# Kernel optimization log

Measured on AMD Instinct MI355X. Metric: run time of the kernel, lower is better.

## Reference

```python
import jax, jax.numpy as jnp
import numpy as np

VOCAB = 50257
D_MODEL = 768
N_LAYERS = 4
N_HEADS = 12
D_HEAD = D_MODEL // N_HEADS
MAX_LEN = 5000
EPS = 1e-5


def _make_pe(max_len, d_model):
    # sinusoidal PE, interleaved sin/cos, base n=10000 (matches PositionalEncodingLayer)
    pos = jnp.arange(max_len, dtype=jnp.float32)[:, None]            # [L,1]
    i = jnp.arange(d_model // 2, dtype=jnp.float32)[None, :]         # [1,D/2]
    theta = pos / jnp.power(10000.0, 2.0 * i / d_model)              # [L,D/2]
    pe = jnp.zeros((max_len, d_model), dtype=jnp.float32)
    pe = pe.at[:, 0::2].set(jnp.sin(theta))
    pe = pe.at[:, 1::2].set(jnp.cos(theta))
    return pe


def setup_inputs() -> dict:
    key = jax.random.key(0)
    ks = jax.random.split(key, 10)
    B, S = 2, 1024
    tokens = jax.random.randint(ks[0], (B, S), 0, VOCAB)
    std = 0.02
    embed = jax.random.normal(ks[1], (VOCAB, D_MODEL), jnp.float32) * std
    pe = _make_pe(MAX_LEN, D_MODEL)
    # per-layer stacked params, torch nn.Linear convention: y = x @ W.T + b
    wq_w = jax.random.normal(ks[2], (N_LAYERS, D_MODEL, D_MODEL), jnp.float32) * std
    wk_w = jax.random.normal(ks[3], (N_LAYERS, D_MODEL, D_MODEL), jnp.float32) * std
    wv_w = jax.random.normal(ks[4], (N_LAYERS, D_MODEL, D_MODEL), jnp.float32) * std
    lin_w = jax.random.normal(ks[5], (N_LAYERS, D_MODEL, D_MODEL), jnp.float32) * std
    wq_b = jnp.zeros((N_LAYERS, D_MODEL), jnp.float32)
    wk_b = jnp.zeros((N_LAYERS, D_MODEL), jnp.float32)
    wv_b = jnp.zeros((N_LAYERS, D_MODEL), jnp.float32)
    lin_b = jnp.zeros((N_LAYERS, D_MODEL), jnp.float32)
    n1_s = jnp.ones((N_LAYERS, D_MODEL), jnp.float32)
    n1_b = jnp.zeros((N_LAYERS, D_MODEL), jnp.float32)
    n2_s = jnp.ones((N_LAYERS, D_MODEL), jnp.float32)
    n2_b = jnp.zeros((N_LAYERS, D_MODEL), jnp.float32)
    unembed_w = jax.random.normal(ks[6], (VOCAB, D_MODEL), jnp.float32) * std
    unembed_b = jnp.zeros((VOCAB,), jnp.float32)
    return dict(tokens=tokens, embed=embed, pe=pe,
                wq_w=wq_w, wq_b=wq_b, wk_w=wk_w, wk_b=wk_b, wv_w=wv_w, wv_b=wv_b,
                lin_w=lin_w, lin_b=lin_b, n1_s=n1_s, n1_b=n1_b, n2_s=n2_s, n2_b=n2_b,
                unembed_w=unembed_w, unembed_b=unembed_b)


def _layernorm(x, scale, bias):
    m = jnp.mean(x, axis=-1, keepdims=True)
    v = jnp.mean(jnp.square(x - m), axis=-1, keepdims=True)
    return (x - m) * jax.lax.rsqrt(v + EPS) * scale + bias


def _attn_block(x, wq_w, wq_b, wk_w, wk_b, wv_w, wv_b, lin_w, lin_b, n1_s, n1_b, n2_s, n2_b):
    B, S, D = x.shape
    def proj(w, b):
        y = x @ w.T + b
        return y.reshape(B, S, N_HEADS, D_HEAD).transpose(0, 2, 1, 3)  # [B,H,S,Dh]
    q, k, v = proj(wq_w, wq_b), proj(wk_w, wk_b), proj(wv_w, wv_b)
    scores = jnp.einsum('bhqd,bhkd->bhqk', q, k) / jnp.sqrt(jnp.float32(D_HEAD))
    causal = jnp.tril(jnp.ones((S, S), dtype=bool))
    scores = jnp.where(causal, scores, -jnp.inf)
    probs = jax.nn.softmax(scores, axis=-1)
    attn = jnp.einsum('bhqk,bhkd->bhqd', probs, v)
    attn = attn.transpose(0, 2, 1, 3).reshape(B, S, D)
    x = _layernorm(x + attn, n1_s, n1_b)
    x = _layernorm(x + (x @ lin_w.T + lin_b), n2_s, n2_b)
    return x


def reference(tokens, embed, pe, wq_w, wq_b, wk_w, wk_b, wv_w, wv_b,
              lin_w, lin_b, n1_s, n1_b, n2_s, n2_b, unembed_w, unembed_b):
    B, S = tokens.shape
    x = embed[tokens] + pe[:S]
    for l in range(N_LAYERS):
        x = _attn_block(x, wq_w[l], wq_b[l], wk_w[l], wk_b[l], wv_w[l], wv_b[l],
                        lin_w[l], lin_b[l], n1_s[l], n1_b[l], n2_s[l], n2_b[l])
    logits = x @ unembed_w.T + unembed_b
    return logits
```

## Files before the change

### kernel.cpp

```cpp
#include <hip/hip_runtime.h>
#include <hip/hip_bf16.h>


#define VOCAB 50257
#define DM 768
#define NL 4
#define NH 12
#define DH 64
#define SEQ 1024
#define BATCH 2
#define ROWS (BATCH * SEQ)
#define QKVN (3 * DM)

typedef __attribute__((ext_vector_type(8))) short short8;
typedef __attribute__((ext_vector_type(4))) float f32x4;

__device__ __forceinline__ unsigned short f2bf(float f) {
    union { float f; unsigned u; } v; v.f = f;
    unsigned r = v.u + 0x7FFFu + ((v.u >> 16) & 1u);
    return (unsigned short)(r >> 16);
}

#define GLOAD16(gp, lp)                                                        \
    __builtin_amdgcn_global_load_lds(                                          \
        (const __attribute__((address_space(1))) unsigned int*)(gp),           \
        (__attribute__((address_space(3))) unsigned int*)(lp), 16, 0, 0)

__global__ __launch_bounds__(256) void cvt_kernel(const float* __restrict__ in,
                                                  unsigned short* __restrict__ out,
                                                  int n4) {
    int i = blockIdx.x * 256 + threadIdx.x;
    if (i < n4) {
        float4 v = ((const float4*)in)[i];
        ushort4 o;
        o.x = f2bf(v.x); o.y = f2bf(v.y); o.z = f2bf(v.z); o.w = f2bf(v.w);
        ((ushort4*)out)[i] = o;
    }
}

__global__ __launch_bounds__(256) void cvt_qkv_kernel(const float* __restrict__ wq,
                                                      const float* __restrict__ wk,
                                                      const float* __restrict__ wv,
                                                      unsigned short* __restrict__ dst,
                                                      int n4) {
    int i = blockIdx.x * 256 + threadIdx.x;
    if (i >= n4) return;
    const int PER_L = 3 * DM * DM / 4, PER_W = DM * DM / 4;
    int l = i / PER_L;
    int rem = i - l * PER_L;
    int w = rem / PER_W;
    int r2 = rem - w * PER_W;
    const float* src = (w == 0) ? wq : (w == 1) ? wk : wv;
    float4 v = ((const float4*)src)[(size_t)l * PER_W + r2];
    ushort4 o;
    o.x = f2bf(v.x); o.y = f2bf(v.y); o.z = f2bf(v.z); o.w = f2bf(v.w);
    ((ushort4*)dst)[i] = o;
}

__global__ __launch_bounds__(256) void pack_qkv_bias(const float* __restrict__ bq,
                                                     const float* __restrict__ bk,
                                                     const float* __restrict__ bv,
                                                     float* __restrict__ dst) {
    int i = blockIdx.x * 256 + threadIdx.x;
    if (i >= NL * QKVN) return;
    int l = i / QKVN, c = i - l * QKVN;
    int w = c / DM, cc = c - w * DM;
    const float* src = (w == 0) ? bq : (w == 1) ? bk : bv;
    dst[i] = src[l * DM + cc];
}

__global__ __launch_bounds__(256) void embed_kernel(const int* __restrict__ tok,
                                                    const float* __restrict__ emb,
                                                    const float* __restrict__ pe,
                                                    float* __restrict__ xf,
                                                    unsigned short* __restrict__ xb) {
    int row = blockIdx.x;
    int t = tok[row];
    int s = row & (SEQ - 1);
    #pragma unroll
    for (int j = 0; j < 3; ++j) {
        int c = threadIdx.x + j * 256;
        float v = emb[(size_t)t * DM + c] + pe[(size_t)s * DM + c];
        xf[(size_t)row * DM + c] = v;
        xb[(size_t)row * DM + c] = f2bf(v);
    }
}

__device__ __forceinline__ float block_sum(float x, float* red) {
    #pragma unroll
    for (int off = 32; off > 0; off >>= 1) x += __shfl_down(x, off);
    int w = threadIdx.x >> 6;
    if ((threadIdx.x & 63) == 0) red[w] = x;
    __syncthreads();
    float t = (red[0] + red[1]) + (red[2] + red[3]);
    __syncthreads();
    return t;
}

__global__ __launch_bounds__(256) void ln_kernel(const float* __restrict__ A,
                                                 const float* __restrict__ Bi,
                                                 const float* __restrict__ sc,
                                                 const float* __restrict__ bi,
                                                 float* __restrict__ xf,
                                                 unsigned short* __restrict__ xb) {
    __shared__ float red[4];
    int row = blockIdx.x, tid = threadIdx.x;
    const float* ap = A + (size_t)row * DM;
    const float* bp = Bi + (size_t)row * DM;
    float v[3], sum = 0.f;
    #pragma unroll
    for (int j = 0; j < 3; ++j) { v[j] = ap[tid + j * 256] + bp[tid + j * 256]; sum += v[j]; }
    sum = block_sum(sum, red);
    float mean = sum * (1.f / DM);
    float vs = 0.f;
    #pragma unroll
    for (int j = 0; j < 3; ++j) { float d = v[j] - mean; vs += d * d; }
    vs = block_sum(vs, red);
    float rstd = rsqrtf(vs * (1.f / DM) + 1e-5f);
    #pragma unroll
    for (int j = 0; j < 3; ++j) {
        int c = tid + j * 256;
        float o = (v[j] - mean) * rstd * sc[c] + bi[c];
        xf[(size_t)row * DM + c] = o;
        xb[(size_t)row * DM + c] = f2bf(o);
    }
}

template <int OUT_BF16>
__global__ __launch_bounds__(256) void gemm128(const unsigned short* __restrict__ A,
                                               const unsigned short* __restrict__ B,
                                               const float* __restrict__ bias,
                                               void* __restrict__ C,
                                               int M, int N, int K, int gx) {
    __shared__ __align__(16) unsigned short As[128 * 64];
    __shared__ __align__(16) unsigned short Bs[128 * 64];
    int bid = blockIdx.x;
    const int nwg = gridDim.x;
    if ((nwg & 7) == 0) {
        int q = nwg >> 3;
        bid = (bid & 7) * q + (bid >> 3);
    }
    const int bx = bid % gx, by = bid / gx;
    const int m0 = bx * 128, n0 = by * 128;
    const int tid = threadIdx.x, lane = tid & 63, wid = tid >> 6;
    const int wm = wid >> 1, wn = wid & 1;
    const int lr = lane & 15, lq = lane >> 4;

    const int sr = wid * 32 + (lane >> 3);
    const int sch = lane & 7;
    const int scs = sch ^ (sr & 7);
    const unsigned short* aP[4];
    const unsigned short* bP[4];
    unsigned short* aL[4];
    unsigned short* bL[4];
    #pragma unroll
    for (int i = 0; i < 4; ++i) {
        int r = sr + i * 8;
        aP[i] = A + (size_t)(m0 + r) * K + scs * 8;
        int br = n0 + r; if (br >= N) br = N - 1;
        bP[i] = B + (size_t)br * K + scs * 8;
        aL[i] = &As[r * 64 + sch * 8];
        bL[i] = &Bs[r * 64 + sch * 8];
    }

    f32x4 acc[4][4] = {};

    for (int k0 = 0; k0 < K; k0 += 64) {
        #pragma unroll
        for (int i = 0; i < 4; ++i) GLOAD16(aP[i] + k0, aL[i]);
        #pragma unroll
        for (int i = 0; i < 4; ++i) GLOAD16(bP[i] + k0, bL[i]);
        __syncthreads();
        #pragma unroll
        for (int kk = 0; kk < 2; ++kk) {
            short8 a[4], b[4];
            #pragma unroll
            for (int i = 0; i < 4; ++i) {
                int ar = wm * 64 + i * 16 + lr;
                a[i] = *reinterpret_cast<const short8*>(
                    &As[ar * 64 + (((kk * 4 + lq) ^ (ar & 7)) * 8)]);
                int br = wn * 64 + i * 16 + lr;
                b[i] = *reinterpret_cast<const short8*>(
                    &Bs[br * 64 + (((kk * 4 + lq) ^ (br & 7)) * 8)]);
            }
            #pragma unroll
            for (int i = 0; i < 4; ++i)
                #pragma unroll
                for (int j = 0; j < 4; ++j)
                    acc[i][j] = __builtin_amdgcn_mfma_f32_16x16x32_bf16(a[i], b[j], acc[i][j], 0, 0, 0);
        }
        __syncthreads();
    }
    #pragma unroll
    for (int i = 0; i < 4; ++i) {
        int row = m0 + wm * 64 + i * 16 + lq * 4;
        #pragma unroll
        for (int j = 0; j < 4; ++j) {
            int col = n0 + wn * 64 + j * 16 + lr;
            if (col < N) {
                float bv = bias[col];
                #pragma unroll
                for (int r = 0; r < 4; ++r) {
                    float v = acc[i][j][r] + bv;
                    if (OUT_BF16) ((unsigned short*)C)[(size_t)(row + r) * N + col] = f2bf(v);
                    else          ((float*)C)[(size_t)(row + r) * N + col] = v;
                }
            }
        }
    }
}

__global__ __launch_bounds__(256) void attn_kernel(const unsigned short* __restrict__ Q,
                                                   const unsigned short* __restrict__ K,
                                                   const unsigned short* __restrict__ V,
                                                   int ld,
                                                   float* __restrict__ O) {
    __shared__ __align__(16) unsigned short Ks[64 * 64];
    __shared__ __align__(16) unsigned short Vs[64 * 64];
    __shared__ __align__(16) unsigned short Ps[4][16 * 64];
    const int qb = blockIdx.x;
    const int bh = blockIdx.y;
    const int b = bh / NH, h = bh % NH;
    const int tid = threadIdx.x, lane = tid & 63, w = tid >> 6;
    const int lr = lane & 15, lq = lane >> 4;
    const int wq0 = qb * 64 + w * 16;
    const size_t base = (size_t)b * SEQ * ld + h * DH;
    const size_t obase = (size_t)b * SEQ * DM + h * DH;

    short8 qf[2];
    {
        const unsigned short* qp = Q + base + (size_t)(wq0 + lr) * ld + lq * 8;
        qf[0] = *reinterpret_cast<const short8*>(qp);
        qf[1] = *reinterpret_cast<const short8*>(qp + 32);
    }
    f32x4 o_acc[4] = {};
    float mrow[4], lrow[4];
    #pragma unroll
    for (int r = 0; r < 4; ++r) { mrow[r] = -1e30f; lrow[r] = 0.f; }

    const int srow = tid >> 3, scol = (tid & 7) * 8;
    for (int t = 0; t <= qb; ++t) {
        const int kv0 = t * 64;
        #pragma unroll
        for (int rr = 0; rr < 2; ++rr) {
            int row = rr * 32 + srow;
            {
                const unsigned short* kp = K + base + (size_t)(kv0 + row) * ld + scol;
                short8 v = *reinterpret_cast<const short8*>(kp);
                *reinterpret_cast<short8*>(&Ks[(row * 64 + scol) ^ ((row & 7) << 3)]) = v;
            }
            {
                const unsigned short* vp = V + base + (size_t)(kv0 + row) * ld + scol;
                short8 v = *reinterpret_cast<const short8*>(vp);
                #pragma unroll
                for (int j = 0; j < 8; ++j) {
                    int d = scol + j;
                    Vs[(d * 64 + row) ^ ((d & 7) << 3)] = (unsigned short)v[j];
                }
            }
        }
        __syncthreads();
        if (kv0 <= wq0 + 15) {
            f32x4 s[4];
            #pragma unroll
            for (int n = 0; n < 4; ++n) {
                int br = n * 16 + lr;
                short8 b0 = *reinterpret_cast<const short8*>(&Ks[(br * 64 + lq * 8) ^ ((br & 7) << 3)]);
                short8 b1 = *reinterpret_cast<const short8*>(&Ks[(br * 64 + 32 + lq * 8) ^ ((br & 7) << 3)]);
                f32x4 z = {};
                z = __builtin_amdgcn_mfma_f32_16x16x32_bf16(qf[0], b0, z, 0, 0, 0);
                z = __builtin_amdgcn_mfma_f32_16x16x32_bf16(qf[1], b1, z, 0, 0, 0);
                s[n] = z;
            }
            const bool diag = (t == qb);
            #pragma unroll
            for (int n = 0; n < 4; ++n)
                #pragma unroll
                for (int r = 0; r < 4; ++r) {
                    float v = s[n][r] * 0.125f;
                    if (diag) {
                        int rg = wq0 + lq * 4 + r;
                        int cg = kv0 + n * 16 + lr;
                        if (cg > rg) v = -1e30f;
                    }
                    s[n][r] = v;
                }
            float f[4];
            #pragma unroll
            for (int r = 0; r < 4; ++r) {
                float mx = fmaxf(fmaxf(s[0][r], s[1][r]), fmaxf(s[2][r], s[3][r]));
                #pragma unroll
                for (int off = 1; off < 16; off <<= 1) mx = fmaxf(mx, __shfl_xor(mx, off));
                float mn = fmaxf(mrow[r], mx);
                f[r] = exp2f((mrow[r] - mn) * 1.44269504f);
                mrow[r] = mn;
            }
            #pragma unroll
            for (int n = 0; n < 4; ++n)
                #pragma unroll
                for (int r = 0; r < 4; ++r)
                    s[n][r] = exp2f((s[n][r] - mrow[r]) * 1.44269504f);
            #pragma unroll
            for (int r = 0; r < 4; ++r) {
                float ls = ((s[0][r] + s[1][r]) + (s[2][r] + s[3][r]));
                #pragma unroll
                for (int off = 1; off < 16; off <<= 1) ls += __shfl_xor(ls, off);
                lrow[r] = lrow[r] * f[r] + ls;
            }
            #pragma unroll
            for (int n = 0; n < 4; ++n)
                #pragma unroll
                for (int r = 0; r < 4; ++r) {
                    int pr = lq * 4 + r, pc = n * 16 + lr;
                    Ps[w][(pr * 64 + pc) ^ ((pr & 7) << 3)] = f2bf(s[n][r]);
                }
            #pragma unroll
            for (int n = 0; n < 4; ++n)
                #pragma unroll
                for (int r = 0; r < 4; ++r) o_acc[n][r] *= f[r];
            #pragma unroll
            for (int kk = 0; kk < 2; ++kk) {
                short8 pa = *reinterpret_cast<const short8*>(
                    &Ps[w][(lr * 64 + kk * 32 + lq * 8) ^ ((lr & 7) << 3)]);
                #pragma unroll
                for (int n = 0; n < 4; ++n) {
                    int vr = n * 16 + lr;
                    short8 bv = *reinterpret_cast<const short8*>(
                        &Vs[(vr * 64 + kk * 32 + lq * 8) ^ ((vr & 7) << 3)]);
                    o_acc[n] = __builtin_amdgcn_mfma_f32_16x16x32_bf16(pa, bv, o_acc[n], 0, 0, 0);
                }
            }
        }
        __syncthreads();
    }
    #pragma unroll
    for (int r = 0; r < 4; ++r) {
        float inv = 1.f / lrow[r];
        int row = wq0 + lq * 4 + r;
        #pragma unroll
        for (int n = 0; n < 4; ++n)
            O[obase + (size_t)row * DM + n * 16 + lr] = o_acc[n][r] * inv;
    }
}

extern "C" void kernel_launch(void* const* d_in, const int* in_sizes, int n_in,
                              void* d_out, int out_size, void* d_ws, size_t ws_size,
                              hipStream_t stream) {
    const int*   tokens   = (const int*)d_in[0];
    const float* embed    = (const float*)d_in[1];
    const float* pe       = (const float*)d_in[2];
    const float* wq_w     = (const float*)d_in[3];
    const float* wq_b     = (const float*)d_in[4];
    const float* wk_w     = (const float*)d_in[5];
    const float* wk_b     = (const float*)d_in[6];
    const float* wv_w     = (const float*)d_in[7];
    const float* wv_b     = (const float*)d_in[8];
    const float* lin_w    = (const float*)d_in[9];
    const float* lin_b    = (const float*)d_in[10];
    const float* n1_s     = (const float*)d_in[11];
    const float* n1_b     = (const float*)d_in[12];
    const float* n2_s     = (const float*)d_in[13];
    const float* n2_b     = (const float*)d_in[14];
    const float* unemb_w  = (const float*)d_in[15];
    const float* unemb_b  = (const float*)d_in[16];

    char* ws = (char*)d_ws;
    size_t off = 0;
    auto carve = [&](size_t bytes) { char* p = ws + off; off += (bytes + 255) & ~(size_t)255; return p; };
    float*          xf     = (float*)carve((size_t)ROWS * DM * 4);
    float*          yb     = (float*)carve((size_t)ROWS * DM * 4);
    unsigned short* xb     = (unsigned short*)carve((size_t)ROWS * DM * 2);
    unsigned short* qkv    = (unsigned short*)carve((size_t)ROWS * QKVN * 2);
    unsigned short* wqkv_h = (unsigned short*)carve((size_t)NL * QKVN * DM * 2);
    unsigned short* lin_h  = (unsigned short*)carve((size_t)NL * DM * DM * 2);
    unsigned short* ue_h   = (unsigned short*)carve((size_t)VOCAB * DM * 2);
    float*          qkvb   = (float*)carve((size_t)NL * QKVN * 4);

    {
        int nq4 = NL * QKVN * DM / 4;
        cvt_qkv_kernel<<<(nq4 + 255) / 256, 256, 0, stream>>>(wq_w, wk_w, wv_w, wqkv_h, nq4);
        int nl4 = NL * DM * DM / 4;
        cvt_kernel<<<(nl4 + 255) / 256, 256, 0, stream>>>(lin_w, lin_h, nl4);
        int nu4 = VOCAB * DM / 4;
        cvt_kernel<<<(nu4 + 255) / 256, 256, 0, stream>>>(unemb_w, ue_h, nu4);
        pack_qkv_bias<<<(NL * QKVN + 255) / 256, 256, 0, stream>>>(wq_b, wk_b, wv_b, qkvb);
    }
    embed_kernel<<<ROWS, 256, 0, stream>>>(tokens, embed, pe, xf, xb);

    const int gx = ROWS / 128;
    for (int l = 0; l < NL; ++l) {
        gemm128<1><<<gx * (QKVN / 128), 256, 0, stream>>>(
            xb, wqkv_h + (size_t)l * QKVN * DM, qkvb + l * QKVN, qkv,
            ROWS, QKVN, DM, gx);
        attn_kernel<<<dim3(SEQ / 64, BATCH * NH), 256, 0, stream>>>(
            qkv, qkv + DM, qkv + 2 * DM, QKVN, yb);
        ln_kernel<<<ROWS, 256, 0, stream>>>(xf, yb, n1_s + l * DM, n1_b + l * DM, xf, xb);
        gemm128<0><<<gx * (DM / 128), 256, 0, stream>>>(
            xb, lin_h + (size_t)l * DM * DM, lin_b + l * DM, yb,
            ROWS, DM, DM, gx);
        ln_kernel<<<ROWS, 256, 0, stream>>>(xf, yb, n2_s + l * DM, n2_b + l * DM, xf, xb);
    }
    const int gyu = (VOCAB + 127) / 128;
    gemm128<0><<<gx * gyu, 256, 0, stream>>>(
        xb, ue_h, unemb_b, (float*)d_out, ROWS, VOCAB, DM, gx);
}
```

Before: 809.3 us.

## Use 256x256-tile, 512-thread GEMM for the unembedding projection

Adds a gemm256 kernel with 256x256 output tiles, 8 waves, double-buffered LDS staging through global_load_lds, and XOR-swizzled LDS reads. It replaces the 128x128 gemm128 launch for the large vocab logits GEMM. Larger tiles raise arithmetic intensity and cut redundant A/B loads on the dominant GEMM. In exchange the kernel uses 128KB of LDS and many accumulator registers, which limits occupancy, and the last N tile wastes more work at the vocab edge.

```diff
diff --git a/kernel.cpp b/kernel.cpp
--- a/kernel.cpp
+++ b/kernel.cpp
@@ -208,6 +208,111 @@
             }
         }
     }
+}
+
+template <int OUT_BF16>
+__global__ __launch_bounds__(512, 2) void gemm256(const unsigned short* __restrict__ A,
+                                                  const unsigned short* __restrict__ B,
+                                                  const float* __restrict__ bias,
+                                                  void* __restrict__ C,
+                                                  int M, int N, int K, int gx) {
+    __shared__ __align__(16) unsigned short As[2][256 * 64];
+    __shared__ __align__(16) unsigned short Bs[2][256 * 64];
+    int bid = blockIdx.x;
+    const int nwg = gridDim.x;
+    if ((nwg & 7) == 0) { int q = nwg >> 3; bid = (bid & 7) * q + (bid >> 3); }
+    const int bx = bid % gx, by = bid / gx;
+    const int m0 = bx * 256, n0 = by * 256;
+    const int tid = threadIdx.x, lane = tid & 63, wid = tid >> 6;
+    const int wm = wid >> 2, wn = wid & 3;
+    const int lr = lane & 15, lq = lane >> 4;
+
+    const int sr = tid >> 3;
+    const int sch = tid & 7;
+    const int scs = sch ^ (sr & 7);
+    const unsigned short* aP[4];
+    const unsigned short* bP[4];
+    #pragma unroll
+    for (int i = 0; i < 4; ++i) {
+        int r = sr + i * 64;
+        aP[i] = A + (size_t)(m0 + r) * K + scs * 8;
+        int br = n0 + r; if (br >= N) br = N - 1;
+        bP[i] = B + (size_t)br * K + scs * 8;
+    }
+
+    #define STAGE256(kt, c)                                                    \
+        do {                                                                   \
+            const int _ko = (kt) * 64;                                         \
+            _Pragma("unroll")                                                  \
+            for (int _i = 0; _i < 4; ++_i)                                     \
+                GLOAD16(aP[_i] + _ko, &As[c][(sr + _i * 64) * 64 + sch * 8]);  \
+            _Pragma("unroll")                                                  \
+            for (int _i = 0; _i < 4; ++_i)                                     \
+                GLOAD16(bP[_i] + _ko, &Bs[c][(sr + _i * 64) * 64 + sch * 8]);  \
+        } while (0)
+
+    f32x4 acc[8][4] = {};
+    const int NT = K >> 6;
+
+    STAGE256(0, 0);
+    STAGE256(1, 1);
+    asm volatile("s_waitcnt vmcnt(8)" ::: "memory");
+    __builtin_amdgcn_s_barrier();
+
+    for (int kt = 0; kt < NT; ++kt) {
+        const int c = kt & 1;
+        #pragma unroll
+        for (int kk = 0; kk < 2; ++kk) {
+            short8 af[8], bf[4];
+            #pragma unroll
+            for (int i = 0; i < 8; ++i) {
+                int ar = wm * 128 + i * 16 + lr;
+                af[i] = *reinterpret_cast<const short8*>(
+                    &As[c][ar * 64 + (((kk * 4 + lq) ^ (ar & 7)) * 8)]);
+            }
+            #pragma unroll
+            for (int j = 0; j < 4; ++j) {
+                int br = wn * 64 + j * 16 + lr;
+                bf[j] = *reinterpret_cast<const short8*>(
+                    &Bs[c][br * 64 + (((kk * 4 + lq) ^ (br & 7)) * 8)]);
+            }
+            __builtin_amdgcn_s_setprio(1);
+            #pragma unroll
+            for (int i = 0; i < 8; ++i)
+                #pragma unroll
+                for (int j = 0; j < 4; ++j)
+                    acc[i][j] = __builtin_amdgcn_mfma_f32_16x16x32_bf16(af[i], bf[j], acc[i][j], 0, 0, 0);
+            __builtin_amdgcn_s_setprio(0);
+        }
+        asm volatile("s_waitcnt lgkmcnt(0)" ::: "memory");
+        __builtin_amdgcn_s_barrier();
+        if (kt + 2 < NT) {
+            STAGE256(kt + 2, c);
+            asm volatile("s_waitcnt vmcnt(8)" ::: "memory");
+        } else if (kt + 2 == NT) {
+            asm volatile("s_waitcnt vmcnt(0)" ::: "memory");
+        }
+        __builtin_amdgcn_s_barrier();
+    }
+
+    #pragma unroll
+    for (int i = 0; i < 8; ++i) {
+        int row = m0 + wm * 128 + i * 16 + lq * 4;
+        #pragma unroll
+        for (int j = 0; j < 4; ++j) {
+            int col = n0 + wn * 64 + j * 16 + lr;
+            if (col < N) {
+                float bv = bias[col];
+                #pragma unroll
+                for (int r = 0; r < 4; ++r) {
+                    float v = acc[i][j][r] + bv;
+                    if (OUT_BF16) ((unsigned short*)C)[(size_t)(row + r) * N + col] = f2bf(v);
+                    else          ((float*)C)[(size_t)(row + r) * N + col] = v;
+                }
+            }
+        }
+    }
+    #undef STAGE256
 }
 
 __global__ __launch_bounds__(256) void attn_kernel(const unsigned short* __restrict__ Q,
@@ -400,7 +505,8 @@
             ROWS, DM, DM, gx);
         ln_kernel<<<ROWS, 256, 0, stream>>>(xf, yb, n2_s + l * DM, n2_b + l * DM, xf, xb);
     }
-    const int gyu = (VOCAB + 127) / 128;
-    gemm128<0><<<gx * gyu, 256, 0, stream>>>(
-        xb, ue_h, unemb_b, (float*)d_out, ROWS, VOCAB, DM, gx);
-}
+    const int gxu = ROWS / 256;
+    const int gyu = (VOCAB + 255) / 256;
+    gemm256<0><<<gxu * gyu, 512, 0, stream>>>(
+        xb, ue_h, unemb_b, (float*)d_out, ROWS, VOCAB, DM, gxu);
+}
```

Measured after the change: 831.1 us. 2.7% more time.

## Use 256x256 eight-wave pipelined GEMM for the unembedding projection

Applied to the files above, without the earlier changes.

Adds a new 256x256-tile GEMM kernel with 512 threads, double-buffered LDS staging through direct global-to-LDS loads, and a hand-scheduled ping-pong of partial tile loads interleaved with MFMA phases using explicit barriers, waitcnts and setprio. The kernel also remaps workgroup IDs across XCDs and writes the fp32 logits with nontemporal stores. It replaces the 128x128 GEMM for the large vocab projection, aiming to raise data reuse and overlap memory with compute. The hand-tuned vmcnt counts and barriers are fragile, and 128 KB of LDS per block limits occupancy.

```diff
diff --git a/kernel.cpp b/kernel.cpp
--- a/kernel.cpp
+++ b/kernel.cpp
@@ -25,6 +25,10 @@
     __builtin_amdgcn_global_load_lds(                                          \
         (const __attribute__((address_space(1))) unsigned int*)(gp),           \
         (__attribute__((address_space(3))) unsigned int*)(lp), 16, 0, 0)
+
+#define BARRIER() asm volatile("s_barrier" ::: "memory")
+#define LGKM0()   asm volatile("s_waitcnt lgkmcnt(0)" ::: "memory")
+#define VMCNT(n)  asm volatile("s_waitcnt vmcnt(" #n ")" ::: "memory")
 
 __global__ __launch_bounds__(256) void cvt_kernel(const float* __restrict__ in,
                                                   unsigned short* __restrict__ out,
@@ -208,6 +212,159 @@
             }
         }
     }
+}
+
+template <int OUT_BF16>
+__global__ __launch_bounds__(512, 2) void gemm256_8p(const unsigned short* __restrict__ A,
+                                                     const unsigned short* __restrict__ B,
+                                                     const float* __restrict__ bias,
+                                                     void* __restrict__ C,
+                                                     int N, int gx) {
+    constexpr int K = 768;
+    constexpr int NT = K / 64;
+    __shared__ __align__(16) unsigned short As[2][256 * 64];
+    __shared__ __align__(16) unsigned short Bs[2][256 * 64];
+    int bid = blockIdx.x;
+    const int nwg = gridDim.x;
+    { int q = nwg >> 3; bid = (bid & 7) * q + (bid >> 3); }
+    const int bx = bid % gx, by = bid / gx;
+    const int m0 = bx * 256, n0 = by * 256;
+    const int tid = threadIdx.x, lane = tid & 63, wid = tid >> 6;
+    const int wm = wid >> 2, wn = wid & 3;
+    const int lr = lane & 15, lq = lane >> 4;
+
+    const int sr = tid >> 3;
+    const int sch = tid & 7;
+    const int scs = sch ^ (sr & 7);
+
+    const unsigned short* aB = A + (size_t)(m0 + sr) * K + scs * 8;
+    const unsigned short* bB[2][2];
+    #pragma unroll
+    for (int jh = 0; jh < 2; ++jh)
+        #pragma unroll
+        for (int i = 0; i < 2; ++i) {
+            int row = ((sr >> 5) + 2 * i) * 64 + jh * 32 + (sr & 31);
+            int br = n0 + row; if (br >= N) br = N - 1;
+            bB[jh][i] = B + (size_t)br * K + scs * 8;
+        }
+
+#define STAGE_A(t, c, ih)                                                      \
+    do { _Pragma("unroll")                                                     \
+        for (int _i = 0; _i < 2; ++_i) {                                       \
+            int _row = _i * 128 + (ih) * 64 + sr;                              \
+            GLOAD16(aB + (size_t)(_i * 128 + (ih) * 64) * K + (t) * 64,        \
+                    &As[c][_row * 64 + sch * 8]);                              \
+        } } while (0)
+#define STAGE_B(t, c, jh)                                                      \
+    do { _Pragma("unroll")                                                     \
+        for (int _i = 0; _i < 2; ++_i) {                                       \
+            int _row = ((sr >> 5) + 2 * _i) * 64 + (jh) * 32 + (sr & 31);      \
+            GLOAD16(bB[jh][_i] + (t) * 64,                                     \
+                    &Bs[c][_row * 64 + sch * 8]);                              \
+        } } while (0)
+#define LDA(D, c, ih)                                                          \
+    do { _Pragma("unroll")                                                     \
+        for (int _i = 0; _i < 4; ++_i) {                                       \
+            int _ar = wm * 128 + (ih) * 64 + _i * 16 + lr;                     \
+            _Pragma("unroll")                                                  \
+            for (int _kk = 0; _kk < 2; ++_kk)                                  \
+                D[_i][_kk] = *reinterpret_cast<const short8*>(                 \
+                    &As[c][_ar * 64 + (((_kk * 4 + lq) ^ (_ar & 7)) * 8)]);    \
+        } } while (0)
+#define LDB(D, c, jh)                                                          \
+    do { _Pragma("unroll")                                                     \
+        for (int _j = 0; _j < 2; ++_j) {                                       \
+            int _br = wn * 64 + (jh) * 32 + _j * 16 + lr;                      \
+            _Pragma("unroll")                                                  \
+            for (int _kk = 0; _kk < 2; ++_kk)                                  \
+                D[_j][_kk] = *reinterpret_cast<const short8*>(                 \
+                    &Bs[c][_br * 64 + (((_kk * 4 + lq) ^ (_br & 7)) * 8)]);    \
+        } } while (0)
+#define MFMA16(BI, BJ, AF, BF)                                                 \
+    do { _Pragma("unroll")                                                     \
+        for (int _i = 0; _i < 4; ++_i) {                                       \
+            _Pragma("unroll")                                                  \
+            for (int _j = 0; _j < 2; ++_j) {                                   \
+                acc[(BI) + _i][(BJ) + _j] = __builtin_amdgcn_mfma_f32_16x16x32_bf16( \
+                    AF[_i][0], BF[_j][0], acc[(BI) + _i][(BJ) + _j], 0, 0, 0); \
+                acc[(BI) + _i][(BJ) + _j] = __builtin_amdgcn_mfma_f32_16x16x32_bf16( \
+                    AF[_i][1], BF[_j][1], acc[(BI) + _i][(BJ) + _j], 0, 0, 0); \
+            }                                                                  \
+        } } while (0)
+
+    short8 afr[4][2], b0f[2][2], b1f[2][2];
+    f32x4 acc[8][4] = {};
+
+    STAGE_A(0, 0, 0); STAGE_B(0, 0, 0); STAGE_A(0, 0, 1); STAGE_B(0, 0, 1);
+    STAGE_A(1, 1, 0); STAGE_B(1, 1, 0); STAGE_A(1, 1, 1); STAGE_B(1, 1, 1);
+    VMCNT(8);
+    BARRIER();
+
+    #pragma unroll
+    for (int t = 0; t < NT; ++t) {
+        const int c = t & 1;
+        LDA(afr, c, 0);
+        LDB(b0f, c, 0);
+        if (t >= 1 && t + 1 < NT) STAGE_A(t + 1, c ^ 1, 1);
+        BARRIER();
+        LGKM0();
+        __builtin_amdgcn_s_setprio(1);
+        MFMA16(0, 0, afr, b0f);
+        __builtin_amdgcn_s_setprio(0);
+        if (t == NT - 1) { VMCNT(0); } else { VMCNT(6); }
+        BARRIER();
+        LDB(b1f, c, 1);
+        if (t >= 1 && t + 1 < NT) STAGE_B(t + 1, c ^ 1, 1);
+        BARRIER();
+        LGKM0();
+        __builtin_amdgcn_s_setprio(1);
+        MFMA16(0, 2, afr, b1f);
+        __builtin_amdgcn_s_setprio(0);
+        BARRIER();
+        LDA(afr, c, 1);
+        if (t + 2 < NT) STAGE_A(t + 2, c, 0);
+        BARRIER();
+        LGKM0();
+        __builtin_amdgcn_s_setprio(1);
+        MFMA16(4, 0, afr, b0f);
+        __builtin_amdgcn_s_setprio(0);
+        BARRIER();
+        if (t + 2 < NT) STAGE_B(t + 2, c, 0);
+        BARRIER();
+        LGKM0();
+        __builtin_amdgcn_s_setprio(1);
+        MFMA16(4, 2, afr, b1f);
+        __builtin_amdgcn_s_setprio(0);
+        if (t + 2 < NT) { VMCNT(8); }
+        else if (t + 2 == NT) { VMCNT(4); }
+        BARRIER();
+    }
+
+    #pragma unroll
+    for (int i = 0; i < 8; ++i) {
+        int row = m0 + wm * 128 + i * 16 + lq * 4;
+        #pragma unroll
+        for (int j = 0; j < 4; ++j) {
+            int col = n0 + wn * 64 + j * 16 + lr;
+            if (col < N) {
+                float bv = bias[col];
+                #pragma unroll
+                for (int r = 0; r < 4; ++r) {
+                    float v = acc[i][j][r] + bv;
+                    if (OUT_BF16)
+                        ((unsigned short*)C)[(size_t)(row + r) * N + col] = f2bf(v);
+                    else
+                        __builtin_nontemporal_store(
+                            v, &((float*)C)[(size_t)(row + r) * N + col]);
+                }
+            }
+        }
+    }
+#undef STAGE_A
+#undef STAGE_B
+#undef LDA
+#undef LDB
+#undef MFMA16
 }
 
 __global__ __launch_bounds__(256) void attn_kernel(const unsigned short* __restrict__ Q,
@@ -400,7 +557,8 @@
             ROWS, DM, DM, gx);
         ln_kernel<<<ROWS, 256, 0, stream>>>(xf, yb, n2_s + l * DM, n2_b + l * DM, xf, xb);
     }
-    const int gyu = (VOCAB + 127) / 128;
-    gemm128<0><<<gx * gyu, 256, 0, stream>>>(
-        xb, ue_h, unemb_b, (float*)d_out, ROWS, VOCAB, DM, gx);
-}
+    const int gxu = ROWS / 256;
+    const int gyu = (VOCAB + 255) / 256;
+    gemm256_8p<0><<<gxu * gyu, 512, 0, stream>>>(
+        xb, ue_h, unemb_b, (float*)d_out, VOCAB, gxu);
+}
```

New measurement: 998.4 us. 1.23x slower.

## Double-buffer GEMM LDS tiles to overlap global loads with MFMA

Applied to the files above, without the earlier changes.

The GEMM now keeps two LDS stages and issues the async global-to-LDS loads for tile t+1 before running the MFMAs on tile t. The per-iteration pair of __syncthreads is replaced by a single vmcnt wait plus s_barrier. It also raises wave priority around the MFMA block and adds a two-block occupancy hint. The goal is to hide global load latency, which dominates the large unembedding GEMM. In exchange LDS use doubles to 64KB per block, which may cap how many blocks fit on a CU.

```diff
diff --git a/kernel.cpp b/kernel.cpp
--- a/kernel.cpp
+++ b/kernel.cpp
@@ -25,6 +25,9 @@
     __builtin_amdgcn_global_load_lds(                                          \
         (const __attribute__((address_space(1))) unsigned int*)(gp),           \
         (__attribute__((address_space(3))) unsigned int*)(lp), 16, 0, 0)
+
+#define BARRIER() asm volatile("s_barrier" ::: "memory")
+#define VMCNT0()  asm volatile("s_waitcnt vmcnt(0)" ::: "memory")
 
 __global__ __launch_bounds__(256) void cvt_kernel(const float* __restrict__ in,
                                                   unsigned short* __restrict__ out,
@@ -127,13 +130,13 @@
 }
 
 template <int OUT_BF16>
-__global__ __launch_bounds__(256) void gemm128(const unsigned short* __restrict__ A,
-                                               const unsigned short* __restrict__ B,
-                                               const float* __restrict__ bias,
-                                               void* __restrict__ C,
-                                               int M, int N, int K, int gx) {
-    __shared__ __align__(16) unsigned short As[128 * 64];
-    __shared__ __align__(16) unsigned short Bs[128 * 64];
+__global__ __launch_bounds__(256, 2) void gemm128db(const unsigned short* __restrict__ A,
+                                                    const unsigned short* __restrict__ B,
+                                                    const float* __restrict__ bias,
+                                                    void* __restrict__ C,
+                                                    int M, int N, int K, int gx) {
+    __shared__ __align__(16) unsigned short As[2][128 * 64];
+    __shared__ __align__(16) unsigned short Bs[2][128 * 64];
     int bid = blockIdx.x;
     const int nwg = gridDim.x;
     if ((nwg & 7) == 0) {
@@ -151,26 +154,35 @@
     const int scs = sch ^ (sr & 7);
     const unsigned short* aP[4];
     const unsigned short* bP[4];
-    unsigned short* aL[4];
-    unsigned short* bL[4];
+    int sO[4];
     #pragma unroll
     for (int i = 0; i < 4; ++i) {
         int r = sr + i * 8;
         aP[i] = A + (size_t)(m0 + r) * K + scs * 8;
         int br = n0 + r; if (br >= N) br = N - 1;
         bP[i] = B + (size_t)br * K + scs * 8;
-        aL[i] = &As[r * 64 + sch * 8];
-        bL[i] = &Bs[r * 64 + sch * 8];
-    }
+        sO[i] = r * 64 + sch * 8;
+    }
+
+#define STG(t, c)                                                              \
+    do { _Pragma("unroll")                                                     \
+        for (int _i = 0; _i < 4; ++_i)                                         \
+            GLOAD16(aP[_i] + (t) * 64, &As[c][sO[_i]]);                        \
+        _Pragma("unroll")                                                      \
+        for (int _i = 0; _i < 4; ++_i)                                         \
+            GLOAD16(bP[_i] + (t) * 64, &Bs[c][sO[_i]]);                        \
+    } while (0)
 
     f32x4 acc[4][4] = {};
-
-    for (int k0 = 0; k0 < K; k0 += 64) {
-        #pragma unroll
-        for (int i = 0; i < 4; ++i) GLOAD16(aP[i] + k0, aL[i]);
-        #pragma unroll
-        for (int i = 0; i < 4; ++i) GLOAD16(bP[i] + k0, bL[i]);
-        __syncthreads();
+    const int NT = K >> 6;
+
+    STG(0, 0);
+    VMCNT0();
+    BARRIER();
+
+    int cur = 0;
+    for (int t = 0; t < NT; ++t) {
+        if (t + 1 < NT) STG(t + 1, cur ^ 1);
         #pragma unroll
         for (int kk = 0; kk < 2; ++kk) {
             short8 a[4], b[4];
@@ -178,19 +190,24 @@
             for (int i = 0; i < 4; ++i) {
                 int ar = wm * 64 + i * 16 + lr;
                 a[i] = *reinterpret_cast<const short8*>(
-                    &As[ar * 64 + (((kk * 4 + lq) ^ (ar & 7)) * 8)]);
+                    &As[cur][ar * 64 + (((kk * 4 + lq) ^ (ar & 7)) * 8)]);
                 int br = wn * 64 + i * 16 + lr;
                 b[i] = *reinterpret_cast<const short8*>(
-                    &Bs[br * 64 + (((kk * 4 + lq) ^ (br & 7)) * 8)]);
-            }
+                    &Bs[cur][br * 64 + (((kk * 4 + lq) ^ (br & 7)) * 8)]);
+            }
+            __builtin_amdgcn_s_setprio(1);
             #pragma unroll
             for (int i = 0; i < 4; ++i)
                 #pragma unroll
                 for (int j = 0; j < 4; ++j)
                     acc[i][j] = __builtin_amdgcn_mfma_f32_16x16x32_bf16(a[i], b[j], acc[i][j], 0, 0, 0);
+            __builtin_amdgcn_s_setprio(0);
         }
-        __syncthreads();
-    }
+        VMCNT0();
+        BARRIER();
+        cur ^= 1;
+    }
+
     #pragma unroll
     for (int i = 0; i < 4; ++i) {
         int row = m0 + wm * 64 + i * 16 + lq * 4;
@@ -208,6 +225,7 @@
             }
         }
     }
+#undef STG
 }
 
 __global__ __launch_bounds__(256) void attn_kernel(const unsigned short* __restrict__ Q,
@@ -389,18 +407,18 @@
 
     const int gx = ROWS / 128;
     for (int l = 0; l < NL; ++l) {
-        gemm128<1><<<gx * (QKVN / 128), 256, 0, stream>>>(
+        gemm128db<1><<<gx * (QKVN / 128), 256, 0, stream>>>(
             xb, wqkv_h + (size_t)l * QKVN * DM, qkvb + l * QKVN, qkv,
             ROWS, QKVN, DM, gx);
         attn_kernel<<<dim3(SEQ / 64, BATCH * NH), 256, 0, stream>>>(
             qkv, qkv + DM, qkv + 2 * DM, QKVN, yb);
         ln_kernel<<<ROWS, 256, 0, stream>>>(xf, yb, n1_s + l * DM, n1_b + l * DM, xf, xb);
-        gemm128<0><<<gx * (DM / 128), 256, 0, stream>>>(
+        gemm128db<0><<<gx * (DM / 128), 256, 0, stream>>>(
             xb, lin_h + (size_t)l * DM * DM, lin_b + l * DM, yb,
             ROWS, DM, DM, gx);
         ln_kernel<<<ROWS, 256, 0, stream>>>(xf, yb, n2_s + l * DM, n2_b + l * DM, xf, xb);
     }
     const int gyu = (VOCAB + 127) / 128;
-    gemm128<0><<<gx * gyu, 256, 0, stream>>>(
+    gemm128db<0><<<gx * gyu, 256, 0, stream>>>(
         xb, ue_h, unemb_b, (float*)d_out, ROWS, VOCAB, DM, gx);
 }
```

After: 865.6 us. +7.0%, slower.
